# Performance work log

Hardware: AMD Instinct MI355X
Metric: run time of the kernel (lower is better)

## Reference

```python
import jax, jax.numpy as jnp
import numpy as np

K = 3          # conv kernel size
PW = 4         # parallel window (pw_height == pw_width)
OC = 128       # out_channels
IC = 128       # in_channels
RANK = 256
STRIDE = PW - K + 1  # 2


def _sdk_weight_map(kernel):
    # kernel: [O, C, K, K] numpy. Concat all (top,left) zero-pad placements into PWxPW.
    O, C, k, _ = kernel.shape
    d = PW - k
    maps = []
    for top in range(d + 1):
        for left in range(d + 1):
            pk = np.zeros((O, C, PW, PW), dtype=kernel.dtype)
            pk[:, :, top:top + k, left:left + k] = kernel
            maps.append(pk.reshape(O, -1))
    return np.concatenate(maps, axis=0)  # [(d+1)^2 * O, C*PW*PW]


def setup_inputs() -> dict:
    rng = np.random.default_rng(0)
    kernel = (rng.standard_normal((OC, IC, K, K)) * 0.05).astype(np.float32)
    W = _sdk_weight_map(kernel)  # [512, 2048]
    u, s, vh = np.linalg.svd(W, full_matrices=False)
    Q = (u[:, :RANK] * s[:RANK]).astype(np.float32)   # u_t @ diag(s_t)
    R = vh[:RANK].astype(np.float32)
    key = jax.random.key(0)
    x = jax.random.normal(key, (32, 128, 64, 64), dtype=jnp.float32)
    return {"x": x, "Q": jnp.asarray(Q), "R": jnp.asarray(R)}


def _slice_and_forward(x, Q, R):
    N, C, H, Wd = x.shape
    s = STRIDE
    pad_v = (H + 2 - PW) % s
    pad_h = (Wd + 2 - PW) % s
    ov = -(-(H + 2 - PW) // s) + 1   # ceil div + 1 (matches math.ceil(...)+1)
    oh = -(-(Wd + 2 - PW) // s) + 1
    xp = jnp.pad(x, ((0, 0), (0, 0), (1, 1 + pad_v), (1, 1 + pad_h)))
    # im2col / unfold: feature layout C slowest, then (i, j) within window -> matches F.unfold
    wins = [xp[:, :, i:i + s * (ov - 1) + 1:s, j:j + s * (oh - 1) + 1:s]
            for i in range(PW) for j in range(PW)]
    patches = jnp.stack(wins, axis=2)                      # [N, C, PW*PW, ov, oh]
    flat = patches.reshape(N, C * PW * PW, ov * oh).transpose(0, 2, 1)  # [N, L, C*PW*PW]
    # F.linear(flat, Q @ R) == (flat @ R^T) @ Q^T  (apply low-rank factors sequentially)
    lin = jnp.einsum('nlr,mr->nlm', jnp.einsum('nlf,rf->nlr', flat, R), Q)  # [N, L, s*s*OC]
    lin = lin.reshape(N, ov, oh, s, s, OC).transpose(0, 1, 3, 2, 4, 5)
    lin = lin.reshape(N, H + pad_v // 2, Wd + pad_h // 2, OC)
    lin = lin.transpose(0, 3, 1, 2)                        # NHWC -> NCHW
    return lin[:, :, :H, :Wd]


def reference(x, Q, R):
    return _slice_and_forward(x, Q, R)
```

## Files before the change

### kernel.cpp

```cpp
#include <hip/hip_runtime.h>
#include <hip/hip_bf16.h>

typedef __attribute__((ext_vector_type(8))) short short8;
typedef __attribute__((ext_vector_type(4))) float f32x4;
typedef unsigned int uint;
typedef __attribute__((ext_vector_type(4))) uint uint4v;

#define AS1 __attribute__((address_space(1)))
#define AS3 __attribute__((address_space(3)))

#define QB_OFF  (1u << 20)
#define XPH_OFF (1310720u)

__device__ __forceinline__ uint bf16r(float f) {
    uint u = __float_as_uint(f);
    u += 0x7FFFu + ((u >> 16) & 1u);
    return u >> 16;
}
__device__ __forceinline__ uint pk2(float lo, float hi) {
    return bf16r(lo) | (bf16r(hi) << 16);
}

__global__ __launch_bounds__(256) void prep_kernel(
    const float* __restrict__ x, const float* __restrict__ Q, const float* __restrict__ R,
    char* __restrict__ Rp4, char* __restrict__ Qp4, char* __restrict__ xph)
{
    const int bid = blockIdx.x, tid = threadIdx.x;
    if (bid < 2048) {
        __shared__ float xt[128 * 65];
        const int n = bid >> 6, h = bid & 63;
        {
            const int c = tid >> 1, half = tid & 1;
            const float4* src = (const float4*)(x + (((size_t)(n * 128 + c) * 64 + h) * 64 + half * 32));
            #pragma unroll
            for (int q = 0; q < 8; ++q) {
                float4 v = src[q];
                float* d = &xt[c * 65 + half * 32 + q * 4];
                d[0] = v.x; d[1] = v.y; d[2] = v.z; d[3] = v.w;
            }
        }
        __syncthreads();
        {
            const int w = tid >> 2, cq = tid & 3;
            uint pw[16];
            #pragma unroll
            for (int m = 0; m < 16; ++m)
                pw[m] = pk2(xt[(cq * 32 + 2 * m) * 65 + w], xt[(cq * 32 + 2 * m + 1) * 65 + w]);
            char* dst = xph + (size_t)n * 1115136 + (size_t)(h + 1) * 16896 + (w + 1) * 256 + cq * 64;
            #pragma unroll
            for (int i = 0; i < 4; ++i) {
                uint4v q4 = { pw[4 * i], pw[4 * i + 1], pw[4 * i + 2], pw[4 * i + 3] };
                *(uint4v*)(dst + i * 16) = q4;
            }
        }
        if (tid < 32) {
            int side = tid >> 4, e = tid & 15;
            uint4v z = {0, 0, 0, 0};
            *(uint4v*)(xph + (size_t)n * 1115136 + (size_t)(h + 1) * 16896 + side * 65 * 256 + e * 16) = z;
        }
        if (h == 0) {
            uint4v z = {0, 0, 0, 0};
            #pragma unroll
            for (int it = 0; it < 9; ++it) {
                int idx = tid + it * 256;
                if (idx < 2112) {
                    int rr = (idx >= 1056) ? 65 : 0;
                    int jj = idx - (rr ? 1056 : 0);
                    int col = jj >> 4, e = jj & 15;
                    *(uint4v*)(xph + (size_t)n * 1115136 + (size_t)rr * 16896 + col * 256 + e * 16) = z;
                }
            }
        }
    } else if (bid < 2304) {
        int g = (bid - 2048) * 256 + tid;
        int s = g >> 10, rem = g & 1023;
        int cu = rem >> 8, col = rem & 255;
        const float* src = R + (size_t)col * 2048 + (((s & 3) * 32 + cu * 8) * 16 + (s >> 2));
        uint pw[4];
        #pragma unroll
        for (int m = 0; m < 4; ++m)
            pw[m] = pk2(src[(2 * m) * 16], src[(2 * m + 1) * 16]);
        uint4v q4 = { pw[0], pw[1], pw[2], pw[3] };
        *(uint4v*)(Rp4 + (size_t)g * 16) = q4;
    } else {
        int g = (bid - 2304) * 256 + tid;
        int ks = g >> 11, p = g & 2047;
        int col = p >> 2, cu = p & 3;
        const float4* s = (const float4*)(Q + (size_t)col * 256 + ks * 32 + cu * 8);
        float4 a = s[0], b = s[1];
        uint4v q4 = { pk2(a.x, a.y), pk2(a.z, a.w), pk2(b.x, b.y), pk2(b.z, b.w) };
        *(uint4v*)(Qp4 + (size_t)ks * 32768 + p * 16) = q4;
    }
}

__global__ __launch_bounds__(512, 2) void fused_kernel(
    const char* __restrict__ xph, const char* __restrict__ Rp4,
    const char* __restrict__ Qp4, float* __restrict__ out)
{
    extern __shared__ __align__(16) char lds[];

    const int blk = blockIdx.x;
    const int b = (blk & 7) * 32 + (blk >> 3);
    const int n = b >> 3, vt = b & 7;
    const int tid = threadIdx.x;
    const int wave = tid >> 6, lane = tid & 63;
    const int lr = lane & 15, kg = lane >> 4;
    const int wm = wave >> 2, wn = wave & 3;

    const char* xbase = xph + (size_t)n * 1115136;
    const int u16 = tid * 16;

    const int xc = (8 * vt + 2 * ((tid >> 5) & 3)) * 16896 + (tid & 31) * 512 + (tid >> 7) * 16;

    const int a0 = kg * 2048 + (wm * 64 + lr) * 16;
    const int b0 = kg * 4096 + (wn * 64 + lr) * 16;

#define STAGE(t_) { \
        __builtin_amdgcn_global_load_lds( \
            (const AS1 void*)(xbase + xc + ((t_) >> 4) * 16896 + (((t_) >> 2) & 3) * 256 + ((t_) & 3) * 64), \
            (AS3 void*)(lds + ((t_) & 3) * 8192 + u16), 16, 0, 0); \
        _Pragma("unroll") for (int q = 0; q < 2; ++q) \
            __builtin_amdgcn_global_load_lds( \
                (const AS1 void*)(Rp4 + (size_t)(t_) * 16384 + q * 8192 + u16), \
                (AS3 void*)(lds + 32768 + ((t_) & 3) * 16384 + q * 8192 + u16), 16, 0, 0); }

#define BAR1 { __builtin_amdgcn_sched_barrier(0); \
        asm volatile("s_barrier\n\ts_waitcnt lgkmcnt(0)" ::: "memory"); \
        __builtin_amdgcn_sched_barrier(0); }
#define BAR(Nstr) { __builtin_amdgcn_sched_barrier(0); \
        asm volatile("s_waitcnt vmcnt(" Nstr ") lgkmcnt(0)\n\ts_barrier" ::: "memory"); \
        __builtin_amdgcn_sched_barrier(0); }

    f32x4 acc[4][4];
    #pragma unroll
    for (int i = 0; i < 4; ++i)
        #pragma unroll
        for (int j = 0; j < 4; ++j) acc[i][j] = (f32x4)0.f;

    STAGE(0) STAGE(1) STAGE(2)
    BAR("6")

    #pragma unroll
    for (int t = 0; t < 64; ++t) {
        if (t <= 60) STAGE(t + 3)
        const char* xs = lds + (t & 3) * 8192;
        const char* bs = lds + 32768 + (t & 3) * 16384;
        short8 af[4], bf[4];
        #pragma unroll
        for (int mf = 0; mf < 4; ++mf)
            af[mf] = *(const short8*)(xs + a0 + mf * 256);
        #pragma unroll
        for (int nf = 0; nf < 4; ++nf)
            bf[nf] = *(const short8*)(bs + b0 + nf * 256);
        BAR1
        __builtin_amdgcn_s_setprio(1);
        #pragma unroll
        for (int nf = 0; nf < 4; ++nf)
            #pragma unroll
            for (int mf = 0; mf < 4; ++mf)
                acc[mf][nf] = __builtin_amdgcn_mfma_f32_16x16x32_bf16(af[mf], bf[nf], acc[mf][nf], 0, 0, 0);
        __builtin_amdgcn_s_setprio(0);
        if (t <= 60)      { BAR("6") }
        else if (t == 61) { BAR("3") }
        else              { BAR("0") }
    }

    {
        const int t0 = (wn * 8 + (lr >> 3)) * 2048 + wm * 1024 + (lr & 7) * 2;
        #pragma unroll
        for (int mf = 0; mf < 4; ++mf)
            #pragma unroll
            for (int nf = 0; nf < 4; ++nf)
                #pragma unroll
                for (int r = 0; r < 4; ++r)
                    *(ushort*)(lds + t0 + nf * 4096 + (mf * 16 + kg * 4 + r) * 16) =
                        (ushort)bf16r(acc[mf][nf][r]);
    }
    __builtin_amdgcn_sched_barrier(0);
    asm volatile("s_waitcnt lgkmcnt(0)\n\ts_barrier" ::: "memory");
    __builtin_amdgcn_sched_barrier(0);

    const int a2 = kg * 2048 + wm * 1024 + lr * 16;
    int qoff[8];
    #pragma unroll
    for (int nf = 0; nf < 8; ++nf)
        qoff[nf] = ((wn >> 1) * 256 + (nf >> 2) * 128 + (wn & 1) * 64 + (nf & 3) * 16 + lr) * 64 + kg * 16;
    const int si = wn >> 1, ochalf = wn & 1;

    f32x4 acc2[4][8];
    #pragma unroll
    for (int i = 0; i < 4; ++i)
        #pragma unroll
        for (int j = 0; j < 8; ++j) acc2[i][j] = (f32x4)0.f;
    #pragma unroll
    for (int ks = 0; ks < 8; ++ks) {
        short8 af2[4];
        #pragma unroll
        for (int mf = 0; mf < 4; ++mf)
            af2[mf] = *(const short8*)(lds + ks * 8192 + a2 + mf * 256);
        #pragma unroll
        for (int nf = 0; nf < 8; ++nf) {
            const short8 bq = *(const short8*)(Qp4 + (size_t)ks * 32768 + qoff[nf]);
            #pragma unroll
            for (int mf = 0; mf < 4; ++mf)
                acc2[mf][nf] = __builtin_amdgcn_mfma_f32_16x16x32_bf16(af2[mf], bq, acc2[mf][nf], 0, 0, 0);
        }
    }

    #pragma unroll
    for (int mf = 0; mf < 4; ++mf) {
        const int h = 8 * vt + 4 * wm + 2 * (mf >> 1) + si;
        float* ob = out + (size_t)n * 524288 + (size_t)h * 64 + (mf & 1) * 32 + kg * 8;
        #pragma unroll
        for (int q = 0; q < 4; ++q) {
            const int oc = ochalf * 64 + q * 16 + lr;
            float* o2 = ob + (size_t)oc * 4096;
            f32x4 v0 = { acc2[mf][q][0], acc2[mf][4 + q][0], acc2[mf][q][1], acc2[mf][4 + q][1] };
            f32x4 v1 = { acc2[mf][q][2], acc2[mf][4 + q][2], acc2[mf][q][3], acc2[mf][4 + q][3] };
            *(f32x4*)(o2) = v0;
            *(f32x4*)(o2 + 4) = v1;
        }
    }
}

extern "C" void kernel_launch(void* const* d_in, const int* in_sizes, int n_in,
                              void* d_out, int out_size, void* d_ws, size_t ws_size,
                              hipStream_t stream) {
    const float* x = (const float*)d_in[0];
    const float* Q = (const float*)d_in[1];
    const float* R = (const float*)d_in[2];
    float* out = (float*)d_out;

    char* ws = (char*)d_ws;
    char* Rp4 = ws;
    char* Qp4 = ws + QB_OFF;
    char* xph = ws + XPH_OFF;

    prep_kernel<<<2368, 256, 0, stream>>>(x, Q, R, Rp4, Qp4, xph);
    fused_kernel<<<256, 512, 98304, stream>>>(xph, Rp4, Qp4, out);
}
```

Measured before the change: 92.46 us.

## Deepen LDS ring to five stages, double-buffer fragments, stage output stores via LDS

The first GEMM's LDS ring buffer grows from four to five stages. Register fragments are double-buffered so the LDS reads for the next step overlap the current MFMAs, and one of the two barriers per iteration is dropped. The epilogue now writes results through a swizzled LDS buffer so each thread stores full contiguous rows to global memory, instead of scattered 32-byte chunks. The cost is more LDS per block (120KB) and more register pressure from the extra fragment set.

Measured after the change: 80.24 us. -13.2%, faster.

```diff
diff --git a/kernel.cpp b/kernel.cpp
--- a/kernel.cpp
+++ b/kernel.cpp
@@ -118,18 +118,30 @@
 #define STAGE(t_) { \
         __builtin_amdgcn_global_load_lds( \
             (const AS1 void*)(xbase + xc + ((t_) >> 4) * 16896 + (((t_) >> 2) & 3) * 256 + ((t_) & 3) * 64), \
-            (AS3 void*)(lds + ((t_) & 3) * 8192 + u16), 16, 0, 0); \
+            (AS3 void*)(lds + ((t_) % 5) * 8192 + u16), 16, 0, 0); \
         _Pragma("unroll") for (int q = 0; q < 2; ++q) \
             __builtin_amdgcn_global_load_lds( \
                 (const AS1 void*)(Rp4 + (size_t)(t_) * 16384 + q * 8192 + u16), \
-                (AS3 void*)(lds + 32768 + ((t_) & 3) * 16384 + q * 8192 + u16), 16, 0, 0); }
-
-#define BAR1 { __builtin_amdgcn_sched_barrier(0); \
-        asm volatile("s_barrier\n\ts_waitcnt lgkmcnt(0)" ::: "memory"); \
-        __builtin_amdgcn_sched_barrier(0); }
-#define BAR(Nstr) { __builtin_amdgcn_sched_barrier(0); \
-        asm volatile("s_waitcnt vmcnt(" Nstr ") lgkmcnt(0)\n\ts_barrier" ::: "memory"); \
-        __builtin_amdgcn_sched_barrier(0); }
+                (AS3 void*)(lds + 40960 + ((t_) % 5) * 16384 + q * 8192 + u16), 16, 0, 0); }
+
+#define FRAGS(af_, bf_, t_) { \
+        const char* xs_ = lds + ((t_) % 5) * 8192; \
+        const char* bs_ = lds + 40960 + ((t_) % 5) * 16384; \
+        _Pragma("unroll") for (int mf = 0; mf < 4; ++mf) \
+            af_[mf] = *(const short8*)(xs_ + a0 + mf * 256); \
+        _Pragma("unroll") for (int nf = 0; nf < 4; ++nf) \
+            bf_[nf] = *(const short8*)(bs_ + b0 + nf * 256); }
+
+#define MFMA16(af_, bf_) { \
+        __builtin_amdgcn_s_setprio(1); \
+        _Pragma("unroll") for (int nf = 0; nf < 4; ++nf) \
+            _Pragma("unroll") for (int mf = 0; mf < 4; ++mf) \
+                acc[mf][nf] = __builtin_amdgcn_mfma_f32_16x16x32_bf16(af_[mf], bf_[nf], acc[mf][nf], 0, 0, 0); \
+        __builtin_amdgcn_s_setprio(0); }
+
+#define SB __builtin_amdgcn_sched_barrier(0);
+#define LGKM(Nstr) { SB asm volatile("s_waitcnt lgkmcnt(" Nstr ")" ::: "memory"); SB }
+#define ENDBAR(Nstr) { SB asm volatile("s_waitcnt vmcnt(" Nstr ")\n\ts_barrier" ::: "memory"); SB }
 
     f32x4 acc[4][4];
     #pragma unroll
@@ -137,33 +149,41 @@
         #pragma unroll
         for (int j = 0; j < 4; ++j) acc[i][j] = (f32x4)0.f;
 
-    STAGE(0) STAGE(1) STAGE(2)
-    BAR("6")
-
-    #pragma unroll
-    for (int t = 0; t < 64; ++t) {
-        if (t <= 60) STAGE(t + 3)
-        const char* xs = lds + (t & 3) * 8192;
-        const char* bs = lds + 32768 + (t & 3) * 16384;
-        short8 af[4], bf[4];
-        #pragma unroll
-        for (int mf = 0; mf < 4; ++mf)
-            af[mf] = *(const short8*)(xs + a0 + mf * 256);
-        #pragma unroll
-        for (int nf = 0; nf < 4; ++nf)
-            bf[nf] = *(const short8*)(bs + b0 + nf * 256);
-        BAR1
-        __builtin_amdgcn_s_setprio(1);
-        #pragma unroll
-        for (int nf = 0; nf < 4; ++nf)
-            #pragma unroll
-            for (int mf = 0; mf < 4; ++mf)
-                acc[mf][nf] = __builtin_amdgcn_mfma_f32_16x16x32_bf16(af[mf], bf[nf], acc[mf][nf], 0, 0, 0);
-        __builtin_amdgcn_s_setprio(0);
-        if (t <= 60)      { BAR("6") }
-        else if (t == 61) { BAR("3") }
-        else              { BAR("0") }
-    }
+    short8 afA[4], bfA[4], afB[4], bfB[4];
+
+    STAGE(0) STAGE(1) STAGE(2) STAGE(3)
+    ENDBAR("6")
+    FRAGS(afA, bfA, 0)
+
+    #pragma unroll
+    for (int p = 0; p < 60; p += 2) {
+        STAGE(p + 4)
+        FRAGS(afB, bfB, p + 1)
+        LGKM("8")
+        MFMA16(afA, bfA)
+        ENDBAR("6")
+        STAGE(p + 5)
+        FRAGS(afA, bfA, p + 2)
+        LGKM("8")
+        MFMA16(afB, bfB)
+        ENDBAR("6")
+    }
+    FRAGS(afB, bfB, 61)
+    LGKM("8")
+    MFMA16(afA, bfA)
+    ENDBAR("3")
+    FRAGS(afA, bfA, 62)
+    LGKM("8")
+    MFMA16(afB, bfB)
+    ENDBAR("0")
+    FRAGS(afB, bfB, 63)
+    LGKM("8")
+    MFMA16(afA, bfA)
+    SB asm volatile("s_barrier" ::: "memory"); SB
+    LGKM("0")
+    MFMA16(afB, bfB)
+
+    __syncthreads();
 
     {
         const int t0 = (wn * 8 + (lr >> 3)) * 2048 + wm * 1024 + (lr & 7) * 2;
@@ -176,9 +196,7 @@
                     *(ushort*)(lds + t0 + nf * 4096 + (mf * 16 + kg * 4 + r) * 16) =
                         (ushort)bf16r(acc[mf][nf][r]);
     }
-    __builtin_amdgcn_sched_barrier(0);
-    asm volatile("s_waitcnt lgkmcnt(0)\n\ts_barrier" ::: "memory");
-    __builtin_amdgcn_sched_barrier(0);
+    __syncthreads();
 
     const int a2 = kg * 2048 + wm * 1024 + lr * 16;
     int qoff[8];
@@ -207,18 +225,33 @@
         }
     }
 
-    #pragma unroll
-    for (int mf = 0; mf < 4; ++mf) {
-        const int h = 8 * vt + 4 * wm + 2 * (mf >> 1) + si;
-        float* ob = out + (size_t)n * 524288 + (size_t)h * 64 + (mf & 1) * 32 + kg * 8;
-        #pragma unroll
-        for (int q = 0; q < 4; ++q) {
-            const int oc = ochalf * 64 + q * 16 + lr;
-            float* o2 = ob + (size_t)oc * 4096;
-            f32x4 v0 = { acc2[mf][q][0], acc2[mf][4 + q][0], acc2[mf][q][1], acc2[mf][4 + q][1] };
-            f32x4 v1 = { acc2[mf][q][2], acc2[mf][4 + q][2], acc2[mf][q][3], acc2[mf][4 + q][3] };
-            *(f32x4*)(o2) = v0;
-            *(f32x4*)(o2 + 4) = v1;
+#define LBAR { SB asm volatile("s_waitcnt lgkmcnt(0)\n\ts_barrier" ::: "memory"); SB }
+    #pragma unroll
+    for (int mh = 0; mh < 4; ++mh) {
+        LBAR
+        if (wm == (mh >> 1)) {
+            #pragma unroll
+            for (int mfh = 0; mfh < 2; ++mfh) {
+                const int mf = (mh & 1) * 2 + mfh;
+                #pragma unroll
+                for (int q = 0; q < 4; ++q) {
+                    const int oc = ochalf * 64 + q * 16 + lr;
+                    const int ub = si * 34816 + oc * 272 + (((4 * mfh + kg) ^ (oc & 7)) << 5);
+                    f32x4 v0 = { acc2[mf][q][0], acc2[mf][4 + q][0], acc2[mf][q][1], acc2[mf][4 + q][1] };
+                    f32x4 v1 = { acc2[mf][q][2], acc2[mf][4 + q][2], acc2[mf][q][3], acc2[mf][4 + q][3] };
+                    *(f32x4*)(lds + ub) = v0;
+                    *(f32x4*)(lds + ub + 16) = v1;
+                }
+            }
+        }
+        LBAR
+        #pragma unroll
+        for (int it = 0; it < 8; ++it) {
+            int uidx = it * 512 + tid;
+            int w4 = uidx & 15, oc = (uidx >> 4) & 127, sie = uidx >> 11;
+            f32x4 v = *(const f32x4*)(lds + sie * 34816 + oc * 272 + ((w4 ^ (2 * (oc & 7))) << 4));
+            *(f32x4*)(out + (size_t)n * 524288 + (size_t)oc * 4096
+                          + (8 * vt + 2 * mh + sie) * 64 + w4 * 4) = v;
         }
     }
 }
@@ -237,5 +270,5 @@
     char* xph = ws + XPH_OFF;
 
     prep_kernel<<<2368, 256, 0, stream>>>(x, Q, R, Rp4, Qp4, xph);
-    fused_kernel<<<256, 512, 98304, stream>>>(xph, Rp4, Qp4, out);
-}
+    fused_kernel<<<256, 512, 122880, stream>>>(xph, Rp4, Qp4, out);
+}
```
